# Optimization experiments

Hardware: AMD Instinct MI355X
Metric: run time of the kernel (lower is better)

## Reference

```python
import jax, jax.numpy as jnp
import numpy as np

N, T = 8192, 1024
CD = 4            # coord dim = 2*d
H, KD, VD = 2, 8, 8
DA = 8            # att_coeff feature dim
AOD = 16          # attention output dim
LAT, OUT = 64, 32


def setup_inputs() -> dict:
    key = jax.random.key(0)
    ks = jax.random.split(key, 16)
    inp = {
        "coord1": jax.random.normal(ks[0], (N, CD), jnp.float32),
        "coord2": jax.random.normal(ks[1], (N, CD), jnp.float32),
        "att_coeff": jax.random.uniform(ks[2], (T, DA), jnp.float32),
        "local_coords": jax.random.normal(ks[3], (N, T, CD), jnp.float32),
        "mask": jax.random.bernoulli(ks[4], 0.5, (N, 1, T)),
    }
    s = 0.1
    inp["wq"] = jax.random.normal(ks[5], (CD, H * KD), jnp.float32) * s
    inp["bq"] = jnp.zeros((H * KD,), jnp.float32)
    inp["wk"] = jax.random.normal(ks[6], (CD, H * KD), jnp.float32) * s
    inp["bk"] = jnp.zeros((H * KD,), jnp.float32)
    inp["wv"] = jax.random.normal(ks[7], (DA, H * VD), jnp.float32) * s
    inp["bv"] = jnp.zeros((H * VD,), jnp.float32)
    inp["wo"] = jax.random.normal(ks[8], (H * VD, AOD), jnp.float32) * s
    inp["bo"] = jnp.zeros((AOD,), jnp.float32)
    inp["w1"] = jax.random.normal(ks[9], (2 * CD + AOD, LAT), jnp.float32) * s
    inp["b1"] = jnp.zeros((LAT,), jnp.float32)
    inp["w2"] = jax.random.normal(ks[10], (LAT, LAT), jnp.float32) * s
    inp["b2"] = jnp.zeros((LAT,), jnp.float32)
    inp["wout"] = jax.random.normal(ks[11], (LAT, OUT), jnp.float32) * s
    inp["bout"] = jnp.zeros((OUT,), jnp.float32)
    return inp


def reference(coord1, coord2, att_coeff, local_coords, mask,
              wq, bq, wk, bk, wv, bv, wo, bo,
              w1, b1, w2, b2, wout, bout):
    # --- masked attention over gathered neighbor coords ---
    q = (coord1 @ wq + bq).reshape(N, H, KD)              # [N,h,kd]
    k = (local_coords @ wk + bk).reshape(N, T, H, KD)     # [N,T,h,kd]
    v = (att_coeff @ wv + bv).reshape(T, H, VD)           # [T,h,vd]
    logits = jnp.einsum('nhd,nThd->nhT', q, k) / jnp.sqrt(
        jnp.asarray(KD, coord1.dtype))                    # [N,h,T]
    logits = jnp.where(mask, logits, -1e30)
    attw = jax.nn.softmax(logits, axis=-1)
    attn = jnp.einsum('nhT,Thd->nhd', attw, v).reshape(N, H * VD)
    att = jnp.exp(-(attn @ wo + bo))                      # [N,AOD]
    # --- small tanh MLP stack ---
    act = jnp.concatenate([coord1, coord2, att], axis=-1) # [N,2*CD+AOD]
    act = jnp.tanh(act @ w1 + b1)
    act = jnp.tanh(act @ w2 + b2)
    return jnp.tanh(act @ wout + bout)                    # [N,OUT]
```

## Files before the change

### kernel.cpp

```cpp
#include <hip/hip_runtime.h>
#include <cstdint>


__device__ __forceinline__ float bflo(uint32_t u) { return __uint_as_float(u << 16); }
__device__ __forceinline__ float bfhi(uint32_t u) { return __uint_as_float(u & 0xFFFF0000u); }
__device__ __forceinline__ uint32_t f2bf(float f) {
    uint32_t x = __float_as_uint(f);
    return (x + 0x7FFFu + ((x >> 16) & 1u)) >> 16;
}
__device__ __forceinline__ float ftanh(float x) {
    float e = __expf(2.0f * x);
    return 1.0f - 2.0f / (e + 1.0f);
}

__global__ __launch_bounds__(512)
void attn_phase1(const float* __restrict__ coord1,
                 const float* __restrict__ att_coeff,
                 const float* __restrict__ local_coords,
                 const void*  __restrict__ maskp,
                 const float* __restrict__ Wq, const float* __restrict__ Bq,
                 const float* __restrict__ Wk, const float* __restrict__ Bk,
                 const float* __restrict__ Wv, const float* __restrict__ Bv,
                 float* __restrict__ ws)
{
    __shared__ uint4    vq[2048];
    __shared__ uint32_t mrow[8][256];

    const int tid  = threadIdx.x;
    const int lane = tid & 63;
    const int wid  = tid >> 6;

    uint4 mm = ((const uint4*)maskp)[tid];
    bool ok = (mm.x <= 1u || mm.x == 0x3F800000u) &&
              (mm.y <= 1u || mm.y == 0x3F800000u) &&
              (mm.z <= 1u || mm.z == 0x3F800000u) &&
              (mm.w <= 1u || mm.w == 0x3F800000u);
    const bool m4 = (__all(ok) != 0);

    #pragma unroll
    for (int tt = 0; tt < 2; ++tt) {
        const int t = tid * 2 + tt;
        const float4 a0 = *(const float4*)(att_coeff + t * 8);
        const float4 a1 = *(const float4*)(att_coeff + t * 8 + 4);
        float vr[16];
        #pragma unroll
        for (int o = 0; o < 16; ++o) {
            vr[o] = Bv[o]
                + a0.x * Wv[o]      + a0.y * Wv[16 + o] + a0.z * Wv[32 + o] + a0.w * Wv[48 + o]
                + a1.x * Wv[64 + o] + a1.y * Wv[80 + o] + a1.z * Wv[96 + o] + a1.w * Wv[112 + o];
        }
        #pragma unroll
        for (int h = 0; h < 2; ++h) {
            const int g  = 2 * t + h;
            const int gs = (g & ~7) | ((g ^ (g >> 3)) & 7);
            uint4 pk;
            pk.x = f2bf(vr[h * 8 + 0]) | (f2bf(vr[h * 8 + 1]) << 16);
            pk.y = f2bf(vr[h * 8 + 2]) | (f2bf(vr[h * 8 + 3]) << 16);
            pk.z = f2bf(vr[h * 8 + 4]) | (f2bf(vr[h * 8 + 5]) << 16);
            pk.w = f2bf(vr[h * 8 + 6]) | (f2bf(vr[h * 8 + 7]) << 16);
            vq[gs] = pk;
        }
    }

    const int n = (blockIdx.x << 3) + wid;

    if (m4) {
        const uint4* wp = (const uint4*)((const uint32_t*)maskp + (size_t)n * 1024) + lane * 4;
        uint4 pk;
        uint32_t b[4];
        #pragma unroll
        for (int j = 0; j < 4; ++j) {
            const uint4 w = wp[j];
            b[j] = (w.x ? 1u : 0u) | ((w.y ? 1u : 0u) << 8) |
                   ((w.z ? 1u : 0u) << 16) | ((w.w ? 1u : 0u) << 24);
        }
        pk.x = b[0]; pk.y = b[1]; pk.z = b[2]; pk.w = b[3];
        *(uint4*)&mrow[wid][lane * 4] = pk;
    } else {
        const uint4 w = ((const uint4*)((const uint8_t*)maskp + (size_t)n * 1024))[lane];
        *(uint4*)&mrow[wid][lane * 4] = w;
    }
    __syncthreads();

    const int g0 = 2 * lane;
    const int bg = (g0 & ~7) | ((g0 ^ (g0 >> 3)) & 7);
    const float rs8 = 0.35355339059327373f;

    float A[2][4], Bs[2];
    {
        const float4 c1 = *(const float4*)(coord1 + n * 4);
        float q[16];
        #pragma unroll
        for (int o = 0; o < 16; ++o)
            q[o] = Bq[o] + c1.x * Wq[o] + c1.y * Wq[16 + o] + c1.z * Wq[32 + o] + c1.w * Wq[48 + o];
        #pragma unroll
        for (int h = 0; h < 2; ++h) {
            #pragma unroll
            for (int c = 0; c < 4; ++c) {
                float s = 0.f;
                #pragma unroll
                for (int d = 0; d < 8; ++d) s += q[h * 8 + d] * Wk[c * 16 + h * 8 + d];
                A[h][c] = s * rs8;
            }
            float s2 = 0.f;
            #pragma unroll
            for (int d = 0; d < 8; ++d) s2 += q[h * 8 + d] * Bk[h * 8 + d];
            Bs[h] = s2 * rs8;
        }
    }

    const float4* lcp = (const float4*)local_coords + (size_t)n * 1024 + lane;
    const int  mword = lane >> 2;
    const int  msh   = (lane & 3) * 8;

    float p[16];
    #pragma unroll
    for (int k = 0; k < 16; ++k) p[k] = 0.f;
    float s0 = 0.f, s1 = 0.f;

    #pragma unroll 2
    for (int i = 0; i < 16; ++i) {
        const float4 lc = lcp[i * 64];
        const uint32_t mw = mrow[wid][mword + 16 * i];
        const bool keep = ((mw >> msh) & 0xFFu) != 0u;
        const float v0 = Bs[0] + lc.x * A[0][0] + lc.y * A[0][1] + lc.z * A[0][2] + lc.w * A[0][3];
        const float v1 = Bs[1] + lc.x * A[1][0] + lc.y * A[1][1] + lc.z * A[1][2] + lc.w * A[1][3];
        const float e0 = keep ? __expf(v0) : 0.f;
        const float e1 = keep ? __expf(v1) : 0.f;
        s0 += e0; s1 += e1;
        const uint4 w0 = vq[(bg + (i << 7))];
        const uint4 w1 = vq[(bg + (i << 7)) ^ 1];
        p[0]  += e0 * bflo(w0.x); p[1]  += e0 * bfhi(w0.x);
        p[2]  += e0 * bflo(w0.y); p[3]  += e0 * bfhi(w0.y);
        p[4]  += e0 * bflo(w0.z); p[5]  += e0 * bfhi(w0.z);
        p[6]  += e0 * bflo(w0.w); p[7]  += e0 * bfhi(w0.w);
        p[8]  += e1 * bflo(w1.x); p[9]  += e1 * bfhi(w1.x);
        p[10] += e1 * bflo(w1.y); p[11] += e1 * bfhi(w1.y);
        p[12] += e1 * bflo(w1.z); p[13] += e1 * bfhi(w1.z);
        p[14] += e1 * bflo(w1.w); p[15] += e1 * bfhi(w1.w);
    }

    #pragma unroll
    for (int s = 32; s; s >>= 1) {
        s0 += __shfl_xor(s0, s, 64);
        s1 += __shfl_xor(s1, s, 64);
    }

    if (s0 == 0.0f) {
        #pragma unroll 2
        for (int i = 0; i < 16; ++i) {
            const uint4 w0 = vq[(bg + (i << 7))];
            const uint4 w1 = vq[(bg + (i << 7)) ^ 1];
            p[0]  += bflo(w0.x); p[1]  += bfhi(w0.x);
            p[2]  += bflo(w0.y); p[3]  += bfhi(w0.y);
            p[4]  += bflo(w0.z); p[5]  += bfhi(w0.z);
            p[6]  += bflo(w0.w); p[7]  += bfhi(w0.w);
            p[8]  += bflo(w1.x); p[9]  += bfhi(w1.x);
            p[10] += bflo(w1.y); p[11] += bfhi(w1.y);
            p[12] += bflo(w1.z); p[13] += bfhi(w1.z);
            p[14] += bflo(w1.w); p[15] += bfhi(w1.w);
        }
        s0 = 1024.0f; s1 = 1024.0f;
    }

    {
        const bool h5 = (lane & 32) != 0;
        #pragma unroll
        for (int k = 0; k < 8; ++k) {
            const float snd = h5 ? p[k] : p[k + 8];
            const float kp  = h5 ? p[k + 8] : p[k];
            p[k] = kp + __shfl_xor(snd, 32, 64);
        }
        const bool h4 = (lane & 16) != 0;
        #pragma unroll
        for (int k = 0; k < 4; ++k) {
            const float snd = h4 ? p[k] : p[k + 4];
            const float kp  = h4 ? p[k + 4] : p[k];
            p[k] = kp + __shfl_xor(snd, 16, 64);
        }
        const bool h3 = (lane & 8) != 0;
        #pragma unroll
        for (int k = 0; k < 2; ++k) {
            const float snd = h3 ? p[k] : p[k + 2];
            const float kp  = h3 ? p[k + 2] : p[k];
            p[k] = kp + __shfl_xor(snd, 8, 64);
        }
        const bool h2 = (lane & 4) != 0;
        {
            const float snd = h2 ? p[0] : p[1];
            const float kp  = h2 ? p[1] : p[0];
            p[0] = kp + __shfl_xor(snd, 4, 64);
        }
        p[0] += __shfl_xor(p[0], 2, 64);
        p[0] += __shfl_xor(p[0], 1, 64);
    }

    if ((lane & 3) == 0)
        ws[(size_t)n * 16 + (lane >> 2)] = p[0] / (lane >= 32 ? s1 : s0);
}

__global__ void attn_phase2(const float* __restrict__ coord1,
                            const float* __restrict__ coord2,
                            const float* __restrict__ ws,
                            const float* __restrict__ Wo, const float* __restrict__ Bo,
                            const float* __restrict__ W1, const float* __restrict__ B1,
                            const float* __restrict__ W2, const float* __restrict__ B2,
                            const float* __restrict__ Wt, const float* __restrict__ Bt,
                            float* __restrict__ out)
{
    const int lane = threadIdx.x & 63;
    const int wid  = threadIdx.x >> 6;
    const int n    = (blockIdx.x << 2) + wid;

    const float4 c1 = *(const float4*)(coord1 + n * 4);
    const float4 c2 = *(const float4*)(coord2 + n * 4);
    const float  av = ws[(size_t)n * 16 + (lane & 15)];

    float attv;
    {
        const int j = lane & 15;
        float acc = Bo[j];
        #pragma unroll
        for (int c = 0; c < 16; ++c)
            acc += __shfl(av, c, 64) * Wo[c * 16 + j];
        attv = __expf(-acc);
    }

    float a1;
    {
        float acc = B1[lane];
        acc += c1.x * W1[0 * 64 + lane] + c1.y * W1[1 * 64 + lane]
             + c1.z * W1[2 * 64 + lane] + c1.w * W1[3 * 64 + lane];
        acc += c2.x * W1[4 * 64 + lane] + c2.y * W1[5 * 64 + lane]
             + c2.z * W1[6 * 64 + lane] + c2.w * W1[7 * 64 + lane];
        #pragma unroll
        for (int c = 0; c < 16; ++c)
            acc += __shfl(attv, c, 64) * W1[(8 + c) * 64 + lane];
        a1 = ftanh(acc);
    }

    float a2;
    {
        float acc = B2[lane];
        #pragma unroll
        for (int c = 0; c < 64; ++c)
            acc += __shfl(a1, c, 64) * W2[c * 64 + lane];
        a2 = ftanh(acc);
    }

    {
        const int j = lane & 31;
        float acc = Bt[j];
        #pragma unroll
        for (int c = 0; c < 64; ++c)
            acc += __shfl(a2, c, 64) * Wt[c * 32 + j];
        if (lane < 32) out[(size_t)n * 32 + lane] = ftanh(acc);
    }
}

extern "C" void kernel_launch(void* const* d_in, const int* in_sizes, int n_in,
                              void* d_out, int out_size, void* d_ws, size_t ws_size,
                              hipStream_t stream) {
    (void)in_sizes; (void)n_in; (void)out_size; (void)ws_size;
    float* ws = (float*)d_ws;
    attn_phase1<<<1024, 512, 0, stream>>>(
        (const float*)d_in[0],  (const float*)d_in[2],
        (const float*)d_in[3],  d_in[4],
        (const float*)d_in[5],  (const float*)d_in[6],
        (const float*)d_in[7],  (const float*)d_in[8],
        (const float*)d_in[9],  (const float*)d_in[10],
        ws);
    attn_phase2<<<2048, 256, 0, stream>>>(
        (const float*)d_in[0],  (const float*)d_in[1],
        ws,
        (const float*)d_in[11], (const float*)d_in[12],
        (const float*)d_in[13], (const float*)d_in[14],
        (const float*)d_in[15], (const float*)d_in[16],
        (const float*)d_in[17], (const float*)d_in[18],
        (float*)d_out);
}
```

Baseline: 58.14 us.

## Split each row's T-loop across two waves and combine partial sums in LDS

Each row of N is now handled by two wavefronts, each covering half of the 1024 neighbors, and the grid is doubled to 2048 blocks. The partial softmax numerators and denominators are combined through a small shared array after an extra barrier. The all-masked fallback now computes the mean of V from att_coeff directly instead of looping over shared memory. This adds parallelism and shortens each wave's serial loop, at the cost of rebuilding the V table in LDS twice as often (once per block) and an additional block-wide sync.

```diff
diff --git a/kernel.cpp b/kernel.cpp
--- a/kernel.cpp
+++ b/kernel.cpp
@@ -24,11 +24,14 @@
                  float* __restrict__ ws)
 {
     __shared__ uint4    vq[2048];
-    __shared__ uint32_t mrow[8][256];
+    __shared__ uint32_t mrow[4][256];
+    __shared__ float    comb[8][20];
 
     const int tid  = threadIdx.x;
     const int lane = tid & 63;
     const int wid  = tid >> 6;
+    const int r    = wid >> 1;
+    const int half = wid & 1;
 
     uint4 mm = ((const uint4*)maskp)[tid];
     bool ok = (mm.x <= 1u || mm.x == 0x3F800000u) &&
@@ -62,23 +65,25 @@
         }
     }
 
-    const int n = (blockIdx.x << 3) + wid;
-
-    if (m4) {
-        const uint4* wp = (const uint4*)((const uint32_t*)maskp + (size_t)n * 1024) + lane * 4;
-        uint4 pk;
-        uint32_t b[4];
-        #pragma unroll
-        for (int j = 0; j < 4; ++j) {
-            const uint4 w = wp[j];
-            b[j] = (w.x ? 1u : 0u) | ((w.y ? 1u : 0u) << 8) |
-                   ((w.z ? 1u : 0u) << 16) | ((w.w ? 1u : 0u) << 24);
-        }
-        pk.x = b[0]; pk.y = b[1]; pk.z = b[2]; pk.w = b[3];
-        *(uint4*)&mrow[wid][lane * 4] = pk;
-    } else {
-        const uint4 w = ((const uint4*)((const uint8_t*)maskp + (size_t)n * 1024))[lane];
-        *(uint4*)&mrow[wid][lane * 4] = w;
+    const int n = (blockIdx.x << 2) + r;
+
+    if (half == 0) {
+        if (m4) {
+            const uint4* wp = (const uint4*)((const uint32_t*)maskp + (size_t)n * 1024) + lane * 4;
+            uint4 pk;
+            uint32_t b[4];
+            #pragma unroll
+            for (int j = 0; j < 4; ++j) {
+                const uint4 w = wp[j];
+                b[j] = (w.x ? 1u : 0u) | ((w.y ? 1u : 0u) << 8) |
+                       ((w.z ? 1u : 0u) << 16) | ((w.w ? 1u : 0u) << 24);
+            }
+            pk.x = b[0]; pk.y = b[1]; pk.z = b[2]; pk.w = b[3];
+            *(uint4*)&mrow[r][lane * 4] = pk;
+        } else {
+            const uint4 w = ((const uint4*)((const uint8_t*)maskp + (size_t)n * 1024))[lane];
+            *(uint4*)&mrow[r][lane * 4] = w;
+        }
     }
     __syncthreads();
 
@@ -112,6 +117,7 @@
     const float4* lcp = (const float4*)local_coords + (size_t)n * 1024 + lane;
     const int  mword = lane >> 2;
     const int  msh   = (lane & 3) * 8;
+    const int  i0    = half * 8;
 
     float p[16];
     #pragma unroll
@@ -119,9 +125,10 @@
     float s0 = 0.f, s1 = 0.f;
 
     #pragma unroll 2
-    for (int i = 0; i < 16; ++i) {
+    for (int ii = 0; ii < 8; ++ii) {
+        const int i = i0 + ii;
         const float4 lc = lcp[i * 64];
-        const uint32_t mw = mrow[wid][mword + 16 * i];
+        const uint32_t mw = mrow[r][mword + 16 * i];
         const bool keep = ((mw >> msh) & 0xFFu) != 0u;
         const float v0 = Bs[0] + lc.x * A[0][0] + lc.y * A[0][1] + lc.z * A[0][2] + lc.w * A[0][3];
         const float v1 = Bs[1] + lc.x * A[1][0] + lc.y * A[1][1] + lc.z * A[1][2] + lc.w * A[1][3];
@@ -146,23 +153,6 @@
         s1 += __shfl_xor(s1, s, 64);
     }
 
-    if (s0 == 0.0f) {
-        #pragma unroll 2
-        for (int i = 0; i < 16; ++i) {
-            const uint4 w0 = vq[(bg + (i << 7))];
-            const uint4 w1 = vq[(bg + (i << 7)) ^ 1];
-            p[0]  += bflo(w0.x); p[1]  += bfhi(w0.x);
-            p[2]  += bflo(w0.y); p[3]  += bfhi(w0.y);
-            p[4]  += bflo(w0.z); p[5]  += bfhi(w0.z);
-            p[6]  += bflo(w0.w); p[7]  += bfhi(w0.w);
-            p[8]  += bflo(w1.x); p[9]  += bfhi(w1.x);
-            p[10] += bflo(w1.y); p[11] += bfhi(w1.y);
-            p[12] += bflo(w1.z); p[13] += bfhi(w1.z);
-            p[14] += bflo(w1.w); p[15] += bfhi(w1.w);
-        }
-        s0 = 1024.0f; s1 = 1024.0f;
-    }
-
     {
         const bool h5 = (lane & 32) != 0;
         #pragma unroll
@@ -195,8 +185,38 @@
         p[0] += __shfl_xor(p[0], 1, 64);
     }
 
-    if ((lane & 3) == 0)
-        ws[(size_t)n * 16 + (lane >> 2)] = p[0] / (lane >= 32 ? s1 : s0);
+    if ((lane & 3) == 0) comb[wid][lane >> 2] = p[0];
+    if (lane == 0) { comb[wid][16] = s0; comb[wid][17] = s1; }
+    __syncthreads();
+
+    if (half == 0) {
+        const float s0T = comb[wid][16] + comb[wid + 1][16];
+        const float s1T = comb[wid][17] + comb[wid + 1][17];
+        if (s0T != 0.0f) {
+            if ((lane & 3) == 0) {
+                const int c = lane >> 2;
+                const float pT = comb[wid][c] + comb[wid + 1][c];
+                ws[(size_t)n * 16 + c] = pT / (c >= 8 ? s1T : s0T);
+            }
+        } else {
+            float meanA[8];
+            #pragma unroll
+            for (int d = 0; d < 8; ++d) {
+                float acc = 0.f;
+                for (int t = lane; t < 1024; t += 64) acc += att_coeff[t * 8 + d];
+                #pragma unroll
+                for (int s = 32; s; s >>= 1) acc += __shfl_xor(acc, s, 64);
+                meanA[d] = acc * (1.0f / 1024.0f);
+            }
+            if ((lane & 3) == 0) {
+                const int c = lane >> 2;
+                float v = Bv[c];
+                #pragma unroll
+                for (int d = 0; d < 8; ++d) v += meanA[d] * Wv[d * 16 + c];
+                ws[(size_t)n * 16 + c] = v;
+            }
+        }
+    }
 }
 
 __global__ void attn_phase2(const float* __restrict__ coord1,
@@ -263,7 +283,7 @@
                               hipStream_t stream) {
     (void)in_sizes; (void)n_in; (void)out_size; (void)ws_size;
     float* ws = (float*)d_ws;
-    attn_phase1<<<1024, 512, 0, stream>>>(
+    attn_phase1<<<2048, 512, 0, stream>>>(
         (const float*)d_in[0],  (const float*)d_in[2],
         (const float*)d_in[3],  d_in[4],
         (const float*)d_in[5],  (const float*)d_in[6],
```

New measurement: 63.29 us. 1.09x slower.
